# Optimization experiments

Measured on AMD Instinct MI355X. Metric: run time of the kernel, lower is better.

## Reference

```python
import jax, jax.numpy as jnp
import numpy as np

# GLIF / surrogate hyperparams (from `params` init kwarg)
ALPHA = 0.5      # synaptic current decay
GAMMA = 0.75     # membrane decay
VTH = 1.0        # base threshold
BADAPT = 0.1     # adaptive-threshold coupling
RHO = 0.9        # adaptation decay
K = 10.0         # fast-sigmoid surrogate slope
T = 8            # spike_ts
B = 128
NC = 9

@jax.custom_vjp
def spike_fn(u):
    return (u > 0.0).astype(u.dtype)

def _spike_fwd(u):
    return (u > 0.0).astype(u.dtype), u

def _spike_bwd(u, g):
    # fast sigmoid surrogate gradient: 1 / (k|u| + 1)^2
    return (g / (K * jnp.abs(u) + 1.0) ** 2,)

spike_fn.defvjp(_spike_fwd, _spike_bwd)

def conv2d(x, w, b, stride):
    y = jax.lax.conv_general_dilated(x, w, (stride, stride), 'VALID',
                                     dimension_numbers=('NCHW', 'OIHW', 'NCHW'))
    return y + b[None, :, None, None]

def group_norm(x, w, b, groups, eps=1e-5):
    shape = x.shape
    N, C = shape[0], shape[1]
    xg = x.reshape(N, groups, -1)
    m = xg.mean(-1, keepdims=True)
    v = xg.var(-1, keepdims=True)
    xn = ((xg - m) * jax.lax.rsqrt(v + eps)).reshape(shape)
    bshape = (1, C) + (1,) * (len(shape) - 2)
    return xn * w.reshape(bshape) + b.reshape(bshape)

def glif(inp, state):
    # current-based generalized LIF with adaptive threshold; state = (i, v, s, a)
    i, v, s, a = state
    i = ALPHA * i + inp
    v = GAMMA * v * (1.0 - s) + i          # multiplicative reset on prior spike
    s_new = spike_fn(v - (VTH + BADAPT * a))
    a = RHO * a + s_new
    return s_new, (i, v, s_new, a)

def mha(tok, wi, bi, wo, bo, n_heads=4):
    Bn, S, E = tok.shape
    d = E // n_heads
    qkv = tok @ wi.T + bi                  # [B,S,3E]
    q, k, v = jnp.split(qkv, 3, axis=-1)
    def heads(t):
        return t.reshape(Bn, S, n_heads, d).transpose(0, 2, 1, 3)
    q, k, v = heads(q), heads(k), heads(v)
    scale = 1.0 / float(d) ** 0.5
    att = jax.nn.softmax(jnp.einsum('bhqd,bhkd->bhqk', q, k) * scale, axis=-1)
    o = jnp.einsum('bhqk,bhkd->bhqd', att, v).transpose(0, 2, 1, 3).reshape(Bn, S, E)
    return o @ wo.T + bo


def setup_inputs() -> dict:
    key = jax.random.key(0)
    ks = jax.random.split(key, 24)
    def n(k, shape, scale=0.05):
        return jax.random.normal(k, shape, jnp.float32) * scale
    return {
        'x': jax.random.uniform(ks[0], (B, 1, 36, 36), jnp.float32),
        'conv0_w': n(ks[1], (64, 1, 7, 7), 0.1), 'conv0_b': n(ks[2], (64,)),
        'gn0_w': jnp.ones((64,), jnp.float32), 'gn0_b': jnp.zeros((64,), jnp.float32),
        'conv1_w': n(ks[3], (64, 64, 7, 7), 0.02), 'conv1_b': n(ks[4], (64,)),
        'gn1_w': jnp.ones((64,), jnp.float32), 'gn1_b': jnp.zeros((64,), jnp.float32),
        'conv2_w': n(ks[5], (64, 64, 7, 7), 0.02), 'conv2_b': n(ks[6], (64,)),
        'gn2_w': jnp.ones((64,), jnp.float32), 'gn2_b': jnp.zeros((64,), jnp.float32),
        'attn_in_w': n(ks[7], (192, 64), 0.1), 'attn_in_b': n(ks[8], (192,)),
        'attn_out_w': n(ks[9], (64, 64), 0.1), 'attn_out_b': n(ks[10], (64,)),
        'fc_w': n(ks[11], (2304, 576), 0.04), 'fc_b': n(ks[12], (2304,)),
        'gnfc_w': jnp.ones((2304,), jnp.float32), 'gnfc_b': jnp.zeros((2304,), jnp.float32),
        'head_w': n(ks[13], (NC, 2304), 0.02), 'head_b': n(ks[14], (NC,)),
        'w_t': jnp.ones((T,), jnp.float32) / T,
    }


def reference(x, conv0_w, conv0_b, gn0_w, gn0_b, conv1_w, conv1_b, gn1_w, gn1_b,
              conv2_w, conv2_b, gn2_w, gn2_b, attn_in_w, attn_in_b, attn_out_w,
              attn_out_b, fc_w, fc_b, gnfc_w, gnfc_b, head_w, head_b, w_t):
    Bn = x.shape[0]
    def zstate(shape):
        z = jnp.zeros((Bn,) + shape, x.dtype)
        return (z, z, z, z)
    init = (zstate((64, 30, 30)), zstate((64, 12, 12)), zstate((64, 3, 3)), zstate((2304,)))

    def step(carry, wt):
        s0, s1, s2, sfc = carry
        h0, s0 = glif(group_norm(conv2d(x, conv0_w, conv0_b, 1), gn0_w, gn0_b, 8), s0)
        h1, s1 = glif(group_norm(conv2d(h0, conv1_w, conv1_b, 2), gn1_w, gn1_b, 8), s1)
        h2, s2 = glif(group_norm(conv2d(h1, conv2_w, conv2_b, 2), gn2_w, gn2_b, 8), s2)
        tok = h2.reshape(Bn, 64, 9).transpose(0, 2, 1)            # [B,9,64]
        tok2 = mha(tok, attn_in_w, attn_in_b, attn_out_w, attn_out_b)
        feat = tok2.transpose(0, 2, 1).reshape(Bn, 64 * 9)        # channel-major flatten
        hf, sfc = glif(group_norm(feat @ fc_w.T + fc_b, gnfc_w, gnfc_b, 32), sfc)
        out = (hf @ head_w.T + head_b) * wt
        return (s0, s1, s2, sfc), out

    _, outs = jax.lax.scan(step, init, w_t)
    return outs.sum(0)
```

## Files before the change

### kernel.cpp

```cpp
#include <hip/hip_runtime.h>
#include <math.h>

__device__ __forceinline__ float np_exp(float x) { return (float)exp((double)x); }

__device__ __forceinline__ float glif_step(float xn, float& ii, float& vv, float& ss, float& aa) {
  ii = __fadd_rn(__fmul_rn(0.5f, ii), xn);
  float vr = __fmul_rn(__fmul_rn(0.75f, vv), __fsub_rn(1.0f, ss));
  vv = __fadd_rn(vr, ii);
  float th = __fadd_rn(1.0f, __fmul_rn(0.1f, aa));
  float u = __fsub_rn(vv, th);
  float ns = u > 0.0f ? 1.0f : 0.0f;
  aa = __fadd_rn(__fmul_rn(0.9f, aa), ns);
  ss = ns;
  return ns;
}

__device__ __forceinline__ float gn_apply(float x, float m, float r, float w, float b) {
  return __fadd_rn(__fmul_rn(__fmul_rn(__fsub_rn(x, m), r), w), b);
}

__global__ __launch_bounds__(64) void f_stats_wave(const float* __restrict__ xsrc,
                                                   float2* __restrict__ mr, int n)
{
  int blk = blockIdx.x;
  int lane = threadIdx.x;
  const float* base = xsrc + (size_t)blk * n;
  double sum = 0.0;
  for (int i = lane; i < n; i += 64) sum += (double)base[i];
  for (int off = 32; off > 0; off >>= 1) sum += __shfl_down(sum, off, 64);
  sum = __shfl(sum, 0, 64);
  float m = (float)(sum / (double)n);
  double sq = 0.0;
  for (int i = lane; i < n; i += 64) {
    float d = __fsub_rn(base[i], m);
    float s2 = __fmul_rn(d, d);
    sq += (double)s2;
  }
  for (int off = 32; off > 0; off >>= 1) sq += __shfl_down(sq, off, 64);
  if (lane == 0) {
    float var = (float)(sq / (double)n);
    float r = __fdiv_rn(1.0f, __fsqrt_rn(__fadd_rn(var, 1e-5f)));
    mr[blk] = make_float2(m, r);
  }
}

__global__ __launch_bounds__(256) void f_stats_serial(const float* __restrict__ xsrc,
                                                      float2* __restrict__ mr, int total)
{
  int gid = blockIdx.x * 256 + threadIdx.x;
  if (gid >= total) return;
  const float* base = xsrc + (size_t)gid * 72;
  double sum = 0.0;
  for (int j = 0; j < 72; j++) sum += (double)base[j];
  float m = (float)(sum / 72.0);
  double sq = 0.0;
  for (int j = 0; j < 72; j++) {
    float d = __fsub_rn(base[j], m);
    float s2 = __fmul_rn(d, d);
    sq += (double)s2;
  }
  float var = (float)(sq / 72.0);
  mr[gid] = make_float2(m, __fdiv_rn(1.0f, __fsqrt_rn(__fadd_rn(var, 1e-5f))));
}

__global__ __launch_bounds__(256) void f_conv0(
    const float* __restrict__ x, const float* __restrict__ w0, const float* __restrict__ b0,
    float* __restrict__ c0)
{
  int gid = blockIdx.x * 256 + threadIdx.x;
  if (gid >= 7372800) return;
  int p = gid % 900;
  int c = (gid / 900) % 64;
  int b = gid / 57600;
  int oy = p / 30, ox = p % 30;
  float acc = 0.0f;
  for (int ky = 0; ky < 7; ky++)
    for (int kx = 0; kx < 7; kx++)
      acc = __fadd_rn(acc, __fmul_rn(w0[c * 49 + ky * 7 + kx],
                                     x[b * 1296 + (oy + ky) * 36 + (ox + kx)]));
  c0[gid] = __fadd_rn(acc, b0[c]);
}

__global__ __launch_bounds__(256) void f_glif0(
    const float* __restrict__ c0, const float2* __restrict__ mr0,
    const float* __restrict__ gnw, const float* __restrict__ gnb, unsigned char* __restrict__ h0)
{
  int gid = blockIdx.x * 256 + threadIdx.x;
  if (gid >= 7372800) return;
  int c = (gid / 900) % 64;
  int b = gid / 57600;
  float2 mrv = mr0[b * 8 + (c >> 3)];
  float xn = gn_apply(c0[gid], mrv.x, mrv.y, gnw[c], gnb[c]);
  float ii = 0.f, vv = 0.f, ss = 0.f, aa = 0.f;
  for (int t = 0; t < 8; t++) {
    float ns = glif_step(xn, ii, vv, ss, aa);
    h0[(size_t)t * 7372800 + gid] = (unsigned char)ns;
  }
}

__global__ __launch_bounds__(256) void f_conv1(
    const unsigned char* __restrict__ h0, const float* __restrict__ w1,
    const float* __restrict__ b1, float* __restrict__ y1)
{
  int tb = blockIdx.x;
  int tid = threadIdx.x;
  __shared__ float sp[7200];
  int ot = tid >> 4;
  int pg = tid & 15;
  int och0 = ot * 4;
  int oy0 = (pg >> 2) * 3;
  int ox0 = (pg & 3) * 3;
  float acc[4][9];
#pragma unroll
  for (int j = 0; j < 4; j++)
#pragma unroll
    for (int p = 0; p < 9; p++) acc[j][p] = 0.0f;

  for (int icc = 0; icc < 8; icc++) {
    int ic0 = icc * 8;
    __syncthreads();
    {
      const unsigned int* src = (const unsigned int*)(h0 + (size_t)tb * 57600 + (size_t)ic0 * 900);
      float4* dst = (float4*)sp;
      for (int i = tid; i < 1800; i += 256) {
        unsigned int u = src[i];
        dst[i] = make_float4((float)(u & 0xFF), (float)((u >> 8) & 0xFF),
                             (float)((u >> 16) & 0xFF), (float)((u >> 24) & 0xFF));
      }
    }
    __syncthreads();
    for (int ic = 0; ic < 8; ic++) {
      const float* wq = w1 + ((size_t)och0 * 64 + ic0 + ic) * 49;
      const float* spc = sp + ic * 900;
#pragma unroll
      for (int ky = 0; ky < 7; ky++) {
        float rowv[3][12];
#pragma unroll
        for (int r = 0; r < 3; r++) {
          const float* rp = spc + (2 * (oy0 + r) + ky) * 30 + 2 * ox0;
#pragma unroll
          for (int d = 0; d < 6; d++) {
            float2 t2 = *(const float2*)(rp + 2 * d);
            rowv[r][2 * d] = t2.x; rowv[r][2 * d + 1] = t2.y;
          }
        }
#pragma unroll
        for (int kx = 0; kx < 7; kx++) {
          float wv[4];
#pragma unroll
          for (int j = 0; j < 4; j++) wv[j] = wq[j * 3136 + ky * 7 + kx];
#pragma unroll
          for (int r = 0; r < 3; r++)
#pragma unroll
            for (int c = 0; c < 3; c++) {
              float sv = rowv[r][kx + 2 * c];
#pragma unroll
              for (int j = 0; j < 4; j++)
                acc[j][r * 3 + c] = __fadd_rn(acc[j][r * 3 + c], __fmul_rn(wv[j], sv));
            }
        }
      }
    }
  }
#pragma unroll
  for (int j = 0; j < 4; j++) {
    int och = och0 + j;
    float bb = b1[och];
#pragma unroll
    for (int r = 0; r < 3; r++)
#pragma unroll
      for (int c = 0; c < 3; c++)
        y1[((size_t)tb * 64 + och) * 144 + (oy0 + r) * 12 + (ox0 + c)] =
            __fadd_rn(acc[j][r * 3 + c], bb);
  }
}

__global__ __launch_bounds__(256) void f_glif1(
    const float* __restrict__ y1, const float2* __restrict__ mr1,
    const float* __restrict__ gnw, const float* __restrict__ gnb, unsigned char* __restrict__ h1)
{
  int gid = blockIdx.x * 256 + threadIdx.x;
  if (gid >= 1179648) return;
  int b = gid / 9216;
  int r = gid % 9216;
  int ch = r / 144;
  int g = ch >> 3;
  float gw = gnw[ch], gb = gnb[ch];
  float ii = 0.f, vv = 0.f, ss = 0.f, aa = 0.f;
  for (int t = 0; t < 8; t++) {
    int tb = t * 128 + b;
    float2 mrv = mr1[tb * 8 + g];
    float xn = gn_apply(y1[(size_t)tb * 9216 + r], mrv.x, mrv.y, gw, gb);
    float ns = glif_step(xn, ii, vv, ss, aa);
    h1[(size_t)tb * 9216 + r] = (unsigned char)ns;
  }
}

__global__ __launch_bounds__(576) void f_conv2(
    const unsigned char* __restrict__ h1, const float* __restrict__ w2,
    const float* __restrict__ b2, float* __restrict__ y2)
{
  int tb = blockIdx.x;
  int tid = threadIdx.x;
  __shared__ float sp[9216];
  {
    const unsigned int* src = (const unsigned int*)(h1 + (size_t)tb * 9216);
    float4* dst = (float4*)sp;
    for (int i = tid; i < 2304; i += 576) {
      unsigned int u = src[i];
      dst[i] = make_float4((float)(u & 0xFF), (float)((u >> 8) & 0xFF),
                           (float)((u >> 16) & 0xFF), (float)((u >> 24) & 0xFF));
    }
  }
  __syncthreads();
  int oc = tid / 9;
  int p = tid % 9;
  int oy = p / 3, ox = p % 3;
  float acc = 0.0f;
  const float* wb = w2 + (size_t)oc * 64 * 49;
  for (int ic = 0; ic < 64; ic++) {
    const float* spc = sp + ic * 144;
    const float* wq = wb + ic * 49;
#pragma unroll
    for (int ky = 0; ky < 7; ky++) {
      const float* rp = spc + (2 * oy + ky) * 12 + 2 * ox;
      float rowv[8];
#pragma unroll
      for (int d = 0; d < 4; d++) {
        float2 t2 = *(const float2*)(rp + 2 * d);
        rowv[2 * d] = t2.x; rowv[2 * d + 1] = t2.y;
      }
#pragma unroll
      for (int kx = 0; kx < 7; kx++)
        acc = __fadd_rn(acc, __fmul_rn(wq[ky * 7 + kx], rowv[kx]));
    }
  }
  y2[(size_t)tb * 576 + oc * 9 + p] = __fadd_rn(acc, b2[oc]);
}

__global__ __launch_bounds__(256) void f_glif2(
    const float* __restrict__ y2, const float2* __restrict__ mr2,
    const float* __restrict__ gnw, const float* __restrict__ gnb, float* __restrict__ h2)
{
  int gid = blockIdx.x * 256 + threadIdx.x;
  if (gid >= 73728) return;
  int b = gid / 576;
  int e = gid % 576;
  int c = e / 9;
  int g = e / 72;
  float gw = gnw[c], gb = gnb[c];
  float ii = 0.f, vv = 0.f, ss = 0.f, aa = 0.f;
  for (int t = 0; t < 8; t++) {
    int tb = t * 128 + b;
    float2 mrv = mr2[tb * 8 + g];
    float xn = gn_apply(y2[(size_t)tb * 576 + e], mrv.x, mrv.y, gw, gb);
    float ns = glif_step(xn, ii, vv, ss, aa);
    h2[(size_t)tb * 576 + e] = ns;
  }
}

__global__ __launch_bounds__(256) void f_mha(
    const float* __restrict__ h2, const float* __restrict__ wi, const float* __restrict__ bi,
    const float* __restrict__ wo, const float* __restrict__ bo, float* __restrict__ feat)
{
  int tb = blockIdx.x;
  int tid = threadIdx.x;
  __shared__ float tokl[576];
  __shared__ float qkvl[1728];
  __shared__ float attl[324];
  __shared__ float obufl[576];
  for (int i = tid; i < 576; i += 256) {
    int c = i / 9, s = i % 9;
    tokl[s * 64 + c] = h2[(size_t)tb * 576 + i];
  }
  __syncthreads();
  for (int o = tid; o < 1728; o += 256) {
    int s = o / 192, j = o % 192;
    const float* wr = wi + j * 64;
    const float* tr = tokl + s * 64;
    float acc = 0.0f;
    for (int c = 0; c < 64; c++) acc = __fmaf_rn(tr[c], wr[c], acc);
    qkvl[o] = __fadd_rn(acc, bi[j]);
  }
  __syncthreads();
  if (tid < 36) {
    int qi = tid % 9;
    int h = tid / 9;
    float lg[9];
    for (int kj = 0; kj < 9; kj++) {
      float acc = 0.0f;
      for (int d = 0; d < 16; d++)
        acc = __fadd_rn(acc, __fmul_rn(qkvl[qi * 192 + h * 16 + d],
                                       qkvl[kj * 192 + 64 + h * 16 + d]));
      lg[kj] = __fmul_rn(acc, 0.25f);
    }
    float mx = lg[0];
    for (int kj = 1; kj < 9; kj++) mx = fmaxf(mx, lg[kj]);
    float ev[9];
    for (int kj = 0; kj < 9; kj++) ev[kj] = np_exp(__fsub_rn(lg[kj], mx));
    float s01 = __fadd_rn(ev[0], ev[1]), s23 = __fadd_rn(ev[2], ev[3]);
    float s45 = __fadd_rn(ev[4], ev[5]), s67 = __fadd_rn(ev[6], ev[7]);
    float sum = __fadd_rn(__fadd_rn(s01, s23), __fadd_rn(s45, s67));
    sum = __fadd_rn(sum, ev[8]);
    for (int kj = 0; kj < 9; kj++)
      attl[h * 81 + qi * 9 + kj] = __fdiv_rn(ev[kj], sum);
  }
  __syncthreads();
  for (int o = tid; o < 576; o += 256) {
    int f = o % 64;
    int s = o / 64;
    int h = f >> 4;
    float acc = 0.0f;
    for (int j = 0; j < 9; j++)
      acc = __fadd_rn(acc, __fmul_rn(attl[h * 81 + s * 9 + j], qkvl[j * 192 + 128 + f]));
    obufl[s * 64 + f] = acc;
  }
  __syncthreads();
  for (int o = tid; o < 576; o += 256) {
    int s = o % 9;
    int e = o / 9;
    float acc = 0.0f;
    for (int f = 0; f < 64; f++)
      acc = __fmaf_rn(obufl[s * 64 + f], wo[e * 64 + f], acc);
    feat[(size_t)tb * 576 + e * 9 + s] = __fadd_rn(acc, bo[e]);
  }
}

__global__ __launch_bounds__(256) void f_fc(
    const float* __restrict__ feat, const float* __restrict__ fw, const float* __restrict__ fb,
    float* __restrict__ yfc)
{
  int mb = blockIdx.x;
  int nb = blockIdx.y;
  int tid = threadIdx.x;
  __shared__ float At[32 * 68];
  __shared__ float Bt[32 * 68];
  int tn = tid >> 4, tm = tid & 15;
  int n4 = tn * 4, m4 = tm * 4;
  float acc[4][4];
#pragma unroll
  for (int i = 0; i < 4; i++)
#pragma unroll
    for (int j = 0; j < 4; j++) acc[i][j] = 0.0f;
  for (int kc = 0; kc < 18; kc++) {
    int k0 = kc * 32;
    __syncthreads();
    for (int l = tid; l < 2048; l += 256) {
      int n = l >> 5, k = l & 31;
      At[k * 68 + n] = feat[(size_t)(nb * 64 + n) * 576 + k0 + k];
      Bt[k * 68 + n] = fw[(size_t)(mb * 64 + n) * 576 + k0 + k];
    }
    __syncthreads();
#pragma unroll 8
    for (int k = 0; k < 32; k++) {
      float av[4], bv[4];
#pragma unroll
      for (int i = 0; i < 4; i++) av[i] = At[k * 68 + n4 + i];
#pragma unroll
      for (int j = 0; j < 4; j++) bv[j] = Bt[k * 68 + m4 + j];
#pragma unroll
      for (int i = 0; i < 4; i++)
#pragma unroll
        for (int j = 0; j < 4; j++) acc[i][j] = __fmaf_rn(av[i], bv[j], acc[i][j]);
    }
  }
#pragma unroll
  for (int i = 0; i < 4; i++) {
    int n = nb * 64 + n4 + i;
    int m = mb * 64 + m4;
#pragma unroll
    for (int j = 0; j < 4; j++)
      yfc[(size_t)n * 2304 + m + j] = __fadd_rn(acc[i][j], fb[m + j]);
  }
}

__global__ __launch_bounds__(256) void f_gliffc(
    const float* __restrict__ yfc, const float2* __restrict__ mrfc,
    const float* __restrict__ gnw, const float* __restrict__ gnb, unsigned char* __restrict__ hf)
{
  int gid = blockIdx.x * 256 + threadIdx.x;
  if (gid >= 294912) return;
  int c = gid % 2304;
  int b = gid / 2304;
  int g = c / 72;
  float gw = gnw[c], gb = gnb[c];
  float ii = 0.f, vv = 0.f, ss = 0.f, aa = 0.f;
  for (int t = 0; t < 8; t++) {
    int tb = t * 128 + b;
    float2 mrv = mrfc[tb * 32 + g];
    float xn = gn_apply(yfc[(size_t)tb * 2304 + c], mrv.x, mrv.y, gw, gb);
    float ns = glif_step(xn, ii, vv, ss, aa);
    hf[(size_t)t * 294912 + (size_t)b * 2304 + c] = (unsigned char)ns;
  }
}

__global__ __launch_bounds__(256) void f_head_t(
    const unsigned char* __restrict__ hf, const float* __restrict__ head_w,
    const float* __restrict__ head_b, const float* __restrict__ wt, float* __restrict__ hbuf)
{
  int gid = blockIdx.x * 256 + threadIdx.x;
  if (gid >= 9216) return;
  int t = gid % 8;
  int nc = (gid / 8) % 9;
  int b = gid / 72;
  const float* wr = head_w + (size_t)nc * 2304;
  const unsigned int* hr = (const unsigned int*)(hf + (size_t)t * 294912 + (size_t)b * 2304);
  float acc = 0.0f;
  for (int c4 = 0; c4 < 576; c4++) {
    unsigned int u = hr[c4];
    int c = c4 * 4;
    acc = __fmaf_rn((float)(u & 0xFF), wr[c], acc);
    acc = __fmaf_rn((float)((u >> 8) & 0xFF), wr[c + 1], acc);
    acc = __fmaf_rn((float)((u >> 16) & 0xFF), wr[c + 2], acc);
    acc = __fmaf_rn((float)((u >> 24) & 0xFF), wr[c + 3], acc);
  }
  float ot = __fadd_rn(acc, head_b[nc]);
  hbuf[gid] = __fmul_rn(ot, wt[t]);
}

__global__ __launch_bounds__(256) void f_head_sum(
    const float* __restrict__ hbuf, float* __restrict__ out)
{
  int gid = blockIdx.x * 256 + threadIdx.x;
  if (gid >= 1152) return;
  float outv = 0.0f;
  for (int t = 0; t < 8; t++) outv = __fadd_rn(outv, hbuf[gid * 8 + t]);
  out[gid] = outv;
}

extern "C" void kernel_launch(void* const* d_in, const int* in_sizes, int n_in,
                              void* d_out, int out_size, void* d_ws, size_t ws_size,
                              hipStream_t stream) {
  (void)in_sizes; (void)n_in; (void)out_size; (void)ws_size;
  const float* x       = (const float*)d_in[0];
  const float* conv0_w = (const float*)d_in[1];
  const float* conv0_b = (const float*)d_in[2];
  const float* gn0_w   = (const float*)d_in[3];
  const float* gn0_b   = (const float*)d_in[4];
  const float* conv1_w = (const float*)d_in[5];
  const float* conv1_b = (const float*)d_in[6];
  const float* gn1_w   = (const float*)d_in[7];
  const float* gn1_b   = (const float*)d_in[8];
  const float* conv2_w = (const float*)d_in[9];
  const float* conv2_b = (const float*)d_in[10];
  const float* gn2_w   = (const float*)d_in[11];
  const float* gn2_b   = (const float*)d_in[12];
  const float* wi      = (const float*)d_in[13];
  const float* bi      = (const float*)d_in[14];
  const float* wo      = (const float*)d_in[15];
  const float* bo      = (const float*)d_in[16];
  const float* fc_w    = (const float*)d_in[17];
  const float* fc_b    = (const float*)d_in[18];
  const float* gnfc_w  = (const float*)d_in[19];
  const float* gnfc_b  = (const float*)d_in[20];
  const float* head_w  = (const float*)d_in[21];
  const float* head_b  = (const float*)d_in[22];
  const float* w_t     = (const float*)d_in[23];

  char* ws = (char*)d_ws;
  unsigned char* h0   = (unsigned char*)(ws);
  float*         c0   = (float*)(ws + 58982400);
  float*         y1   = (float*)(ws + 88473600);
  unsigned char* h1   = (unsigned char*)(ws + 126222336);
  float*         y2   = (float*)(ws + 135659520);
  float*         h2   = (float*)(ws + 138018816);
  float*         feat = (float*)(ws + 69746688);
  float*         yfc  = (float*)(ws + 72105984);
  unsigned char* hf   = (unsigned char*)(ws + 81543168);
  float2*        mr0  = (float2*)(ws + 151142400);
  float2*        mr1  = (float2*)(ws + 151150592);
  float2*        mr2  = (float2*)(ws + 151216128);
  float2*        mrfc = (float2*)(ws + 151281664);
  float*         hbuf = (float*)(ws + 151543808);

  f_conv0<<<28800, 256, 0, stream>>>(x, conv0_w, conv0_b, c0);
  f_stats_wave<<<1024, 64, 0, stream>>>(c0, mr0, 7200);
  f_glif0<<<28800, 256, 0, stream>>>(c0, mr0, gn0_w, gn0_b, h0);
  f_conv1<<<1024, 256, 0, stream>>>(h0, conv1_w, conv1_b, y1);
  f_stats_wave<<<8192, 64, 0, stream>>>(y1, mr1, 1152);
  f_glif1<<<4608, 256, 0, stream>>>(y1, mr1, gn1_w, gn1_b, h1);
  f_conv2<<<1024, 576, 0, stream>>>(h1, conv2_w, conv2_b, y2);
  f_stats_serial<<<32, 256, 0, stream>>>(y2, mr2, 8192);
  f_glif2<<<288, 256, 0, stream>>>(y2, mr2, gn2_w, gn2_b, h2);
  f_mha<<<1024, 256, 0, stream>>>(h2, wi, bi, wo, bo, feat);
  dim3 gfc(36, 16);
  f_fc<<<gfc, 256, 0, stream>>>(feat, fc_w, fc_b, yfc);
  f_stats_serial<<<128, 256, 0, stream>>>(yfc, mrfc, 32768);
  f_gliffc<<<1152, 256, 0, stream>>>(yfc, mrfc, gnfc_w, gnfc_b, hf);
  f_head_t<<<36, 256, 0, stream>>>(hf, head_w, head_b, w_t, hbuf);
  f_head_sum<<<5, 256, 0, stream>>>(hbuf, (float*)d_out);
}
```

Before: 1.690 ms.

## Pack layer-0 spikes into row bitmasks and make conv1 a sparse weight-add

The GLIF0 kernel now writes each 30-pixel row of binary spikes as a 32-bit mask per timestep instead of one byte per pixel. conv1 loads the whole 64-channel bitmask plane into shared memory once and, for each output, walks the set bits of the 7-wide window with ffs, adding weights directly with no multiply-accumulate. This cuts spike storage and bandwidth by 8x, drops the chunked shared-memory staging and its barriers, and skips work wherever there is no spike. In exchange, the data-dependent while loop causes wave divergence and serial, uncoalesced weight loads, and glif0 now runs far fewer threads, each handling a full row.

```diff
diff --git a/kernel.cpp b/kernel.cpp
--- a/kernel.cpp
+++ b/kernel.cpp
@@ -81,30 +81,47 @@
   c0[gid] = __fadd_rn(acc, b0[c]);
 }
 
-__global__ __launch_bounds__(256) void f_glif0(
+__global__ __launch_bounds__(256) void f_glif0_bits(
     const float* __restrict__ c0, const float2* __restrict__ mr0,
-    const float* __restrict__ gnw, const float* __restrict__ gnb, unsigned char* __restrict__ h0)
-{
-  int gid = blockIdx.x * 256 + threadIdx.x;
-  if (gid >= 7372800) return;
-  int c = (gid / 900) % 64;
-  int b = gid / 57600;
+    const float* __restrict__ gnw, const float* __restrict__ gnb,
+    unsigned int* __restrict__ h0m)
+{
+  int gid = blockIdx.x * 256 + threadIdx.x;
+  if (gid >= 245760) return;
+  int oy = gid % 30;
+  int c = (gid / 30) % 64;
+  int b = gid / 1920;
   float2 mrv = mr0[b * 8 + (c >> 3)];
-  float xn = gn_apply(c0[gid], mrv.x, mrv.y, gnw[c], gnb[c]);
-  float ii = 0.f, vv = 0.f, ss = 0.f, aa = 0.f;
-  for (int t = 0; t < 8; t++) {
-    float ns = glif_step(xn, ii, vv, ss, aa);
-    h0[(size_t)t * 7372800 + gid] = (unsigned char)ns;
-  }
+  float gw = gnw[c], gb = gnb[c];
+  const float* src = c0 + (size_t)b * 57600 + (size_t)c * 900 + oy * 30;
+  unsigned int m[8] = {0u, 0u, 0u, 0u, 0u, 0u, 0u, 0u};
+  for (int xp = 0; xp < 30; xp++) {
+    float xn = gn_apply(src[xp], mrv.x, mrv.y, gw, gb);
+    float ii = 0.f, vv = 0.f, ss = 0.f, aa = 0.f;
+#pragma unroll
+    for (int t = 0; t < 8; t++) {
+      float ns = glif_step(xn, ii, vv, ss, aa);
+      m[t] |= (ns > 0.5f ? 1u : 0u) << xp;
+    }
+  }
+  size_t base = (size_t)b * 1920 + (size_t)c * 30 + oy;
+#pragma unroll
+  for (int t = 0; t < 8; t++) h0m[(size_t)t * 245760 + base] = m[t];
 }
 
 __global__ __launch_bounds__(256) void f_conv1(
-    const unsigned char* __restrict__ h0, const float* __restrict__ w1,
+    const unsigned int* __restrict__ h0m, const float* __restrict__ w1,
     const float* __restrict__ b1, float* __restrict__ y1)
 {
   int tb = blockIdx.x;
   int tid = threadIdx.x;
-  __shared__ float sp[7200];
+  __shared__ unsigned int lm[1920];
+  {
+    int t = tb / 128, b = tb % 128;
+    const unsigned int* src = h0m + (size_t)t * 245760 + (size_t)b * 1920;
+    for (int i = tid; i < 1920; i += 256) lm[i] = src[i];
+  }
+  __syncthreads();
   int ot = tid >> 4;
   int pg = tid & 15;
   int och0 = ot * 4;
@@ -116,48 +133,27 @@
 #pragma unroll
     for (int p = 0; p < 9; p++) acc[j][p] = 0.0f;
 
-  for (int icc = 0; icc < 8; icc++) {
-    int ic0 = icc * 8;
-    __syncthreads();
-    {
-      const unsigned int* src = (const unsigned int*)(h0 + (size_t)tb * 57600 + (size_t)ic0 * 900);
-      float4* dst = (float4*)sp;
-      for (int i = tid; i < 1800; i += 256) {
-        unsigned int u = src[i];
-        dst[i] = make_float4((float)(u & 0xFF), (float)((u >> 8) & 0xFF),
-                             (float)((u >> 16) & 0xFF), (float)((u >> 24) & 0xFF));
-      }
-    }
-    __syncthreads();
-    for (int ic = 0; ic < 8; ic++) {
-      const float* wq = w1 + ((size_t)och0 * 64 + ic0 + ic) * 49;
-      const float* spc = sp + ic * 900;
-#pragma unroll
-      for (int ky = 0; ky < 7; ky++) {
-        float rowv[3][12];
-#pragma unroll
-        for (int r = 0; r < 3; r++) {
-          const float* rp = spc + (2 * (oy0 + r) + ky) * 30 + 2 * ox0;
-#pragma unroll
-          for (int d = 0; d < 6; d++) {
-            float2 t2 = *(const float2*)(rp + 2 * d);
-            rowv[r][2 * d] = t2.x; rowv[r][2 * d + 1] = t2.y;
+  for (int ic = 0; ic < 64; ic++) {
+    const float* wq = w1 + ((size_t)och0 * 64 + ic) * 49;
+    const unsigned int* lr = lm + ic * 30;
+#pragma unroll
+    for (int ky = 0; ky < 7; ky++) {
+      unsigned int rb[3];
+#pragma unroll
+      for (int r = 0; r < 3; r++) rb[r] = lr[2 * (oy0 + r) + ky];
+      const float* wk = wq + ky * 7;
+#pragma unroll
+      for (int r = 0; r < 3; r++) {
+#pragma unroll
+        for (int cc = 0; cc < 3; cc++) {
+          unsigned int w7 = (rb[r] >> (2 * (ox0 + cc))) & 0x7Fu;
+          while (w7) {
+            int kx = __ffs(w7) - 1;
+            w7 &= w7 - 1;
+#pragma unroll
+            for (int j = 0; j < 4; j++)
+              acc[j][r * 3 + cc] = __fadd_rn(acc[j][r * 3 + cc], wk[j * 3136 + kx]);
           }
-        }
-#pragma unroll
-        for (int kx = 0; kx < 7; kx++) {
-          float wv[4];
-#pragma unroll
-          for (int j = 0; j < 4; j++) wv[j] = wq[j * 3136 + ky * 7 + kx];
-#pragma unroll
-          for (int r = 0; r < 3; r++)
-#pragma unroll
-            for (int c = 0; c < 3; c++) {
-              float sv = rowv[r][kx + 2 * c];
-#pragma unroll
-              for (int j = 0; j < 4; j++)
-                acc[j][r * 3 + c] = __fadd_rn(acc[j][r * 3 + c], __fmul_rn(wv[j], sv));
-            }
         }
       }
     }
@@ -458,7 +454,7 @@
   const float* w_t     = (const float*)d_in[23];
 
   char* ws = (char*)d_ws;
-  unsigned char* h0   = (unsigned char*)(ws);
+  unsigned int*  h0m  = (unsigned int*)(ws);
   float*         c0   = (float*)(ws + 58982400);
   float*         y1   = (float*)(ws + 88473600);
   unsigned char* h1   = (unsigned char*)(ws + 126222336);
@@ -475,8 +471,8 @@
 
   f_conv0<<<28800, 256, 0, stream>>>(x, conv0_w, conv0_b, c0);
   f_stats_wave<<<1024, 64, 0, stream>>>(c0, mr0, 7200);
-  f_glif0<<<28800, 256, 0, stream>>>(c0, mr0, gn0_w, gn0_b, h0);
-  f_conv1<<<1024, 256, 0, stream>>>(h0, conv1_w, conv1_b, y1);
+  f_glif0_bits<<<960, 256, 0, stream>>>(c0, mr0, gn0_w, gn0_b, h0m);
+  f_conv1<<<1024, 256, 0, stream>>>(h0m, conv1_w, conv1_b, y1);
   f_stats_wave<<<8192, 64, 0, stream>>>(y1, mr1, 1152);
   f_glif1<<<4608, 256, 0, stream>>>(y1, mr1, gn1_w, gn1_b, h1);
   f_conv2<<<1024, 576, 0, stream>>>(h1, conv2_w, conv2_b, y2);
```

New measurement: 3.760 ms. 123% more time.
